# Optimization experiments

Measured on AMD Instinct MI355X. Metric: run time of the kernel, lower is better.

## Reference

```python
import jax, jax.numpy as jnp
import numpy as np

N_CB, VOCAB, CDIM = 8, 1024, 16
DECAY = 0.99
EPS = 1e-5


def setup_inputs() -> dict:
    key = jax.random.key(0)
    k1, k2, k3 = jax.random.split(key, 3)
    z = jax.random.normal(k1, (8, N_CB * CDIM, 32, 32), jnp.float32)
    codebooks = jax.random.normal(k2, (N_CB, VOCAB, CDIM), jnp.float32) * 0.02
    ema_count = jnp.zeros((N_CB, VOCAB), jnp.float32)
    ema_weight = jax.random.normal(k3, (N_CB, VOCAB, CDIM), jnp.float32) * 0.02
    return {"z": z, "codebooks": codebooks, "ema_count": ema_count, "ema_weight": ema_weight}


def reference(z, codebooks, ema_count, ema_weight):
    B, D, H, W = z.shape
    # (b d h w) -> (b h w, n_cb, cdim): matches rearrange + chunk(dim=-1)
    zp = z.transpose(0, 2, 3, 1).reshape(B * H * W, N_CB, CDIM)
    # squared distances (N, C, V): |z|^2 - 2 z.cb + |cb|^2
    d2 = (jnp.sum(zp * zp, axis=-1, keepdims=True)
          - 2.0 * jnp.einsum('ncd,cvd->ncv', zp, codebooks)
          + jnp.sum(codebooks * codebooks, axis=-1)[None, :, :])
    idx = jnp.argmin(d2, axis=-1)                      # (N, C) int
    zq = codebooks[jnp.arange(N_CB)[None, :], idx]     # (N, C, d) gather

    # --- EMA codebook update (training-mode math, no grad) ---
    idx_c = idx.T                                      # (C, N)
    zp_c = zp.transpose(1, 0, 2)                       # (C, N, d)
    counts = jax.vmap(lambda i: jnp.zeros((VOCAB,), jnp.float32).at[i].add(1.0))(idx_c)
    sums = jax.vmap(lambda i, x: jnp.zeros((VOCAB, CDIM), jnp.float32).at[i].add(x))(idx_c, zp_c)
    new_count = DECAY * ema_count + (1.0 - DECAY) * counts
    new_weight = DECAY * ema_weight + (1.0 - DECAY) * sums
    n = jnp.sum(new_count, axis=-1, keepdims=True)     # (C, 1)
    count = (new_count + EPS) / (n + VOCAB * EPS) * n  # Laplace-smoothed counts
    new_codebooks = new_weight / count[..., None]

    # commitment: mean over codebooks of per-part MSE == global MSE (equal part sizes)
    commitment = jnp.mean((zp - jax.lax.stop_gradient(zq)) ** 2)

    # straight-through estimator
    zq_st = zp + jax.lax.stop_gradient(zq - zp)        # (N, C, d)
    quantized = zq_st.reshape(B, H, W, D).transpose(0, 3, 1, 2)
    indices = idx.reshape(B, H, W, N_CB).transpose(0, 3, 1, 2)  # (B, C, H, W)
    return quantized, indices, commitment, new_codebooks, new_count, new_weight
```

## Files before the change

### kernel.cpp

```cpp
#include <hip/hip_runtime.h>


#define NCB   8
#define VOCAB 1024
#define CDIM  16
#define NPIX  8192
#define HW    1024

#define OFF_QUANT  0
#define OFF_IDX    1048576
#define OFF_COMMIT 1114112
#define OFF_NCB    1114113
#define OFF_NCNT   1245185
#define OFF_NWT    1253377

#define WS_COUNTS_OFF 0
#define WS_SUMS_OFF   (NCB * VOCAB)
#define WS_CARR_OFF   (NCB * VOCAB + NCB * VOCAB * CDIM)

__device__ __forceinline__ float npsum16(const float m[16]) {
#pragma clang fp contract(off)
  float r0 = m[0] + m[8];
  float r1 = m[1] + m[9];
  float r2 = m[2] + m[10];
  float r3 = m[3] + m[11];
  float r4 = m[4] + m[12];
  float r5 = m[5] + m[13];
  float r6 = m[6] + m[14];
  float r7 = m[7] + m[15];
  return ((r0 + r1) + (r2 + r3)) + ((r4 + r5) + (r6 + r7));
}

__device__ __forceinline__ float npsum16sq(const float a[16]) {
#pragma clang fp contract(off)
  float m[16];
#pragma unroll
  for (int d = 0; d < 16; ++d) m[d] = a[d] * a[d];
  return npsum16(m);
}

__device__ __forceinline__ void proc_entry(const float zv[16],
                                           const float e[16], float c2v,
                                           float z2, int idx, float& best,
                                           int& bi) {
#pragma clang fp contract(off)
  float m[16];
#pragma unroll
  for (int d = 0; d < 16; ++d) m[d] = zv[d] * e[d];
  float l0 = (m[0] + m[4]) + (m[8] + m[12]);
  float l1 = (m[1] + m[5]) + (m[9] + m[13]);
  float l2 = (m[2] + m[6]) + (m[10] + m[14]);
  float l3 = (m[3] + m[7]) + (m[11] + m[15]);
  const float dot = (l0 + l1) + (l2 + l3);
  const float d2 = (z2 - 2.0f * dot) + c2v;
  const bool lt = d2 < best;
  best = lt ? d2 : best;
  bi = lt ? idx : bi;
}

__global__ __launch_bounds__(512, 4) void k_assign(
    const float* __restrict__ z, const float* __restrict__ cb,
    float* __restrict__ out, float* __restrict__ ws_commit_arr) {
  __shared__ float s_c2[VOCAB];
  __shared__ float s_best[8 * 64];
  __shared__ int s_bi[8 * 64];

  const int c = blockIdx.x >> 7;
  const int pchunk = blockIdx.x & 127;
  const int t = threadIdx.x;
  const int pix = t & 63;
  const int w = t >> 6;
  const int wu = __builtin_amdgcn_readfirstlane(w);

  const float* cbc = cb + (size_t)c * VOCAB * CDIM;

  for (int v = t; v < VOCAB; v += 512) {
    float e[16];
#pragma unroll
    for (int d = 0; d < 16; ++d) e[d] = cbc[(size_t)v * CDIM + d];
    s_c2[v] = npsum16sq(e);
  }

  const int n = pchunk * 64 + pix;
  const int b = n >> 10;
  const int hw = n & 1023;

  const float* zbase = z + ((size_t)(b * 128 + c * 16)) * HW + hw;
  float zv[16];
#pragma unroll
  for (int d = 0; d < 16; ++d) zv[d] = zbase[(size_t)d * HW];

  const float z2 = npsum16sq(zv);

  __syncthreads();

  const int vbase = wu * 128;
  const float* ep = cbc + (size_t)vbase * CDIM;

  float best = INFINITY;
  int bi = 0;

#pragma unroll 2
  for (int k = 0; k < 128; k += 2) {
    float ea[16], eb[16];
#pragma unroll
    for (int d = 0; d < 16; ++d) ea[d] = ep[(size_t)k * CDIM + d];
#pragma unroll
    for (int d = 0; d < 16; ++d) eb[d] = ep[(size_t)(k + 1) * CDIM + d];
    const float cv0 = s_c2[vbase + k];
    const float cv1 = s_c2[vbase + k + 1];
    proc_entry(zv, ea, cv0, z2, vbase + k, best, bi);
    proc_entry(zv, eb, cv1, z2, vbase + k + 1, best, bi);
  }

  s_best[w * 64 + pix] = best;
  s_bi[w * 64 + pix] = bi;
  __syncthreads();

  if (t < 64) {
    best = s_best[t];
    bi = s_bi[t];
#pragma unroll
    for (int s = 1; s < 8; ++s) {
      const float ob = s_best[s * 64 + t];
      const int oi = s_bi[s * 64 + t];
      const bool take = (ob < best) || (ob == best && oi < bi);
      best = take ? ob : best;
      bi = take ? oi : bi;
    }

    const float* qe = cbc + (size_t)bi * CDIM;
    float comm = 0.f;
#pragma unroll
    for (int d = 0; d < 16; ++d) {
      float zq = qe[d];
      float diff, qst;
      {
#pragma clang fp contract(off)
        diff = zv[d] - zq;
        qst = zv[d] + (zq - zv[d]);
      }
      comm += diff * diff;
      out[OFF_QUANT + ((size_t)(b * 128 + c * 16 + d)) * HW + hw] = qst;
    }
    out[OFF_IDX + ((size_t)(b * NCB + c)) * HW + hw] = (float)bi;

#pragma unroll
    for (int off = 32; off; off >>= 1) comm += __shfl_down(comm, off);
    if (t == 0) ws_commit_arr[blockIdx.x] = comm;
  }
}

__global__ __launch_bounds__(1024) void k_stats(
    const float* __restrict__ z, const float* __restrict__ outbuf,
    float* __restrict__ ws_counts, float* __restrict__ ws_sums_t) {
  __shared__ float s_sum[VOCAB];
  __shared__ float s_cnt[VOCAB];
  const int c = blockIdx.x >> 4;
  const int d = blockIdx.x & 15;
  const int t = threadIdx.x;

  s_sum[t] = 0.f;
  if (d == 0) s_cnt[t] = 0.f;
  __syncthreads();

#pragma unroll
  for (int k = 0; k < 8; ++k) {
    const int bi = (int)outbuf[OFF_IDX + ((size_t)(k * NCB + c)) * HW + t];
    const float zval = z[((size_t)(k * 128 + c * 16 + d)) * HW + t];
    atomicAdd(&s_sum[bi], zval);
    if (d == 0) atomicAdd(&s_cnt[bi], 1.0f);
  }
  __syncthreads();

  ws_sums_t[((size_t)(c * CDIM + d)) * VOCAB + t] = s_sum[t];
  if (d == 0) ws_counts[c * VOCAB + t] = s_cnt[t];
}

__global__ __launch_bounds__(256) void k_update(
    const float* __restrict__ ema_count, const float* __restrict__ ema_weight,
    const float* __restrict__ ws_counts, const float* __restrict__ ws_sums_t,
    const float* __restrict__ ws_commit_arr, float* __restrict__ out) {
  const int c = blockIdx.x >> 3;
  const int part = blockIdx.x & 7;
  const int t = threadIdx.x;
  __shared__ float s_red[4];
  __shared__ float s_n;
  __shared__ double s_dred[4];

  float psum = 0.f;
#pragma unroll
  for (int k = 0; k < 4; ++k) {
    const int v = k * 256 + t;
    psum += 0.99f * ema_count[c * VOCAB + v] + 0.01f * ws_counts[c * VOCAB + v];
  }
#pragma unroll
  for (int off = 32; off; off >>= 1) psum += __shfl_down(psum, off);
  if ((t & 63) == 0) s_red[t >> 6] = psum;
  __syncthreads();
  if (t == 0) s_n = (s_red[0] + s_red[1]) + (s_red[2] + s_red[3]);
  __syncthreads();
  const float nsum = s_n;
  const float veps = 0.01024f;

  if (t < 128) {
    const int v = part * 128 + t;
    out[OFF_NCNT + c * VOCAB + v] =
        0.99f * ema_count[c * VOCAB + v] + 0.01f * ws_counts[c * VOCAB + v];
  }

#pragma unroll
  for (int k = 0; k < 8; ++k) {
    const int i = part * 2048 + k * 256 + t;
    const int v = i >> 4;
    const int d = i & 15;
    const float nc =
        0.99f * ema_count[c * VOCAB + v] + 0.01f * ws_counts[c * VOCAB + v];
    const float cnt = (nc + 1e-5f) / (nsum + veps) * nsum;
    const size_t gi = (size_t)c * VOCAB * CDIM + i;
    const float nw = 0.99f * ema_weight[gi] +
                     0.01f * ws_sums_t[((size_t)(c * CDIM + d)) * VOCAB + v];
    out[OFF_NWT + gi] = nw;
    out[OFF_NCB + gi] = nw / cnt;
  }

  if (blockIdx.x == 0) {
    double ps = 0.0;
#pragma unroll
    for (int k = 0; k < 4; ++k) ps += (double)ws_commit_arr[k * 256 + t];
#pragma unroll
    for (int off = 32; off; off >>= 1) ps += __shfl_down(ps, off);
    if ((t & 63) == 0) s_dred[t >> 6] = ps;
    __syncthreads();
    if (t == 0)
      out[OFF_COMMIT] =
          (float)(((s_dred[0] + s_dred[1]) + (s_dred[2] + s_dred[3])) /
                  1048576.0);
  }
}

extern "C" void kernel_launch(void* const* d_in, const int* in_sizes, int n_in,
                              void* d_out, int out_size, void* d_ws,
                              size_t ws_size, hipStream_t stream) {
  const float* z = (const float*)d_in[0];
  const float* codebooks = (const float*)d_in[1];
  const float* ema_count = (const float*)d_in[2];
  const float* ema_weight = (const float*)d_in[3];
  float* out = (float*)d_out;

  float* wsf = (float*)d_ws;
  float* ws_counts = wsf + WS_COUNTS_OFF;
  float* ws_sums_t = wsf + WS_SUMS_OFF;
  float* ws_commit_arr = wsf + WS_CARR_OFF;


  k_assign<<<dim3(1024), dim3(512), 0, stream>>>(z, codebooks, out,
                                                 ws_commit_arr);
  k_stats<<<dim3(128), dim3(1024), 0, stream>>>(z, out, ws_counts, ws_sums_t);
  k_update<<<dim3(64), dim3(256), 0, stream>>>(ema_count, ema_weight,
                                               ws_counts, ws_sums_t,
                                               ws_commit_arr, out);
}
```

Before: 143.8 us.

## Fuse histogram statistics and EMA update into one per-codebook kernel

Merges the stats and update kernels into a single kernel with one 1024-thread block per codebook. Each block builds counts and all 16 per-dimension sums in LDS, padded to a stride of 17 to reduce bank conflicts, then applies the EMA update directly from shared memory. This removes one kernel launch and the workspace round trip for counts and sums. In exchange, the work that used to be spread over 128 and 64 blocks now runs on only 8 blocks. Each block serially performs many LDS atomics and streams a large share of z, which could lengthen the tail.

Measured after the change: 300.1 us. 109% more time.

```diff
diff --git a/kernel.cpp b/kernel.cpp
--- a/kernel.cpp
+++ b/kernel.cpp
@@ -14,9 +14,7 @@
 #define OFF_NCNT   1245185
 #define OFF_NWT    1253377
 
-#define WS_COUNTS_OFF 0
-#define WS_SUMS_OFF   (NCB * VOCAB)
-#define WS_CARR_OFF   (NCB * VOCAB + NCB * VOCAB * CDIM)
+#define WS_CARR_OFF 0
 
 __device__ __forceinline__ float npsum16(const float m[16]) {
 #pragma clang fp contract(off)
@@ -151,91 +149,92 @@
   }
 }
 
-__global__ __launch_bounds__(1024) void k_stats(
+__global__ __launch_bounds__(1024) void k_statsupd(
     const float* __restrict__ z, const float* __restrict__ outbuf,
-    float* __restrict__ ws_counts, float* __restrict__ ws_sums_t) {
-  __shared__ float s_sum[VOCAB];
+    const float* __restrict__ ema_count, const float* __restrict__ ema_weight,
+    const float* __restrict__ ws_commit_arr, float* __restrict__ out) {
+  __shared__ float s_sum[VOCAB * 17];
   __shared__ float s_cnt[VOCAB];
-  const int c = blockIdx.x >> 4;
-  const int d = blockIdx.x & 15;
+  __shared__ float s_fred[16];
+  __shared__ float s_n;
+  __shared__ double s_dred[16];
+
+  const int c = blockIdx.x;
   const int t = threadIdx.x;
-
-  s_sum[t] = 0.f;
-  if (d == 0) s_cnt[t] = 0.f;
-  __syncthreads();
-
+  const int lane = t & 63;
+  const int wv = t >> 6;
+
+#pragma unroll
+  for (int j = 0; j < 17; ++j) s_sum[j * 1024 + t] = 0.f;
+  s_cnt[t] = 0.f;
+  __syncthreads();
+
+  int bidx[8];
+#pragma unroll
+  for (int k = 0; k < 8; ++k)
+    bidx[k] = (int)outbuf[OFF_IDX + ((size_t)(k * NCB + c)) * HW + t];
+
+  float zA[16], zB[16];
+#pragma unroll
+  for (int d = 0; d < 16; ++d) zA[d] = z[((size_t)(c * 16 + d)) * HW + t];
 #pragma unroll
   for (int k = 0; k < 8; ++k) {
-    const int bi = (int)outbuf[OFF_IDX + ((size_t)(k * NCB + c)) * HW + t];
-    const float zval = z[((size_t)(k * 128 + c * 16 + d)) * HW + t];
-    atomicAdd(&s_sum[bi], zval);
-    if (d == 0) atomicAdd(&s_cnt[bi], 1.0f);
-  }
-  __syncthreads();
-
-  ws_sums_t[((size_t)(c * CDIM + d)) * VOCAB + t] = s_sum[t];
-  if (d == 0) ws_counts[c * VOCAB + t] = s_cnt[t];
-}
-
-__global__ __launch_bounds__(256) void k_update(
-    const float* __restrict__ ema_count, const float* __restrict__ ema_weight,
-    const float* __restrict__ ws_counts, const float* __restrict__ ws_sums_t,
-    const float* __restrict__ ws_commit_arr, float* __restrict__ out) {
-  const int c = blockIdx.x >> 3;
-  const int part = blockIdx.x & 7;
-  const int t = threadIdx.x;
-  __shared__ float s_red[4];
-  __shared__ float s_n;
-  __shared__ double s_dred[4];
-
-  float psum = 0.f;
-#pragma unroll
-  for (int k = 0; k < 4; ++k) {
-    const int v = k * 256 + t;
-    psum += 0.99f * ema_count[c * VOCAB + v] + 0.01f * ws_counts[c * VOCAB + v];
-  }
+    if (k < 7) {
+#pragma unroll
+      for (int d = 0; d < 16; ++d)
+        zB[d] = z[((size_t)((k + 1) * 128 + c * 16 + d)) * HW + t];
+    }
+    const int bi = bidx[k];
+    atomicAdd(&s_cnt[bi], 1.0f);
+#pragma unroll
+    for (int d = 0; d < 16; ++d) atomicAdd(&s_sum[bi * 17 + d], zA[d]);
+#pragma unroll
+    for (int d = 0; d < 16; ++d) zA[d] = zB[d];
+  }
+  __syncthreads();
+
+  const float ncv = 0.99f * ema_count[c * VOCAB + t] + 0.01f * s_cnt[t];
+  out[OFF_NCNT + c * VOCAB + t] = ncv;
+  float psum = ncv;
 #pragma unroll
   for (int off = 32; off; off >>= 1) psum += __shfl_down(psum, off);
-  if ((t & 63) == 0) s_red[t >> 6] = psum;
-  __syncthreads();
-  if (t == 0) s_n = (s_red[0] + s_red[1]) + (s_red[2] + s_red[3]);
+  if (lane == 0) s_fred[wv] = psum;
+  __syncthreads();
+  if (t == 0) {
+    float s = 0.f;
+#pragma unroll
+    for (int i = 0; i < 16; ++i) s += s_fred[i];
+    s_n = s;
+  }
   __syncthreads();
   const float nsum = s_n;
   const float veps = 0.01024f;
 
-  if (t < 128) {
-    const int v = part * 128 + t;
-    out[OFF_NCNT + c * VOCAB + v] =
-        0.99f * ema_count[c * VOCAB + v] + 0.01f * ws_counts[c * VOCAB + v];
-  }
-
-#pragma unroll
-  for (int k = 0; k < 8; ++k) {
-    const int i = part * 2048 + k * 256 + t;
+#pragma unroll
+  for (int j = 0; j < 16; ++j) {
+    const int i = j * 1024 + t;
     const int v = i >> 4;
     const int d = i & 15;
-    const float nc =
-        0.99f * ema_count[c * VOCAB + v] + 0.01f * ws_counts[c * VOCAB + v];
+    const float nc = 0.99f * ema_count[c * VOCAB + v] + 0.01f * s_cnt[v];
     const float cnt = (nc + 1e-5f) / (nsum + veps) * nsum;
     const size_t gi = (size_t)c * VOCAB * CDIM + i;
-    const float nw = 0.99f * ema_weight[gi] +
-                     0.01f * ws_sums_t[((size_t)(c * CDIM + d)) * VOCAB + v];
+    const float nw = 0.99f * ema_weight[gi] + 0.01f * s_sum[v * 17 + d];
     out[OFF_NWT + gi] = nw;
     out[OFF_NCB + gi] = nw / cnt;
   }
 
-  if (blockIdx.x == 0) {
-    double ps = 0.0;
-#pragma unroll
-    for (int k = 0; k < 4; ++k) ps += (double)ws_commit_arr[k * 256 + t];
+  if (c == 0) {
+    double ps = (double)ws_commit_arr[t];
 #pragma unroll
     for (int off = 32; off; off >>= 1) ps += __shfl_down(ps, off);
-    if ((t & 63) == 0) s_dred[t >> 6] = ps;
+    if (lane == 0) s_dred[wv] = ps;
     __syncthreads();
-    if (t == 0)
-      out[OFF_COMMIT] =
-          (float)(((s_dred[0] + s_dred[1]) + (s_dred[2] + s_dred[3])) /
-                  1048576.0);
+    if (t == 0) {
+      double sd = 0.0;
+#pragma unroll
+      for (int i = 0; i < 16; ++i) sd += s_dred[i];
+      out[OFF_COMMIT] = (float)(sd / 1048576.0);
+    }
   }
 }
 
@@ -248,16 +247,12 @@
   const float* ema_weight = (const float*)d_in[3];
   float* out = (float*)d_out;
 
-  float* wsf = (float*)d_ws;
-  float* ws_counts = wsf + WS_COUNTS_OFF;
-  float* ws_sums_t = wsf + WS_SUMS_OFF;
-  float* ws_commit_arr = wsf + WS_CARR_OFF;
+  float* ws_commit_arr = (float*)d_ws + WS_CARR_OFF;
 
 
   k_assign<<<dim3(1024), dim3(512), 0, stream>>>(z, codebooks, out,
                                                  ws_commit_arr);
-  k_stats<<<dim3(128), dim3(1024), 0, stream>>>(z, out, ws_counts, ws_sums_t);
-  k_update<<<dim3(64), dim3(256), 0, stream>>>(ema_count, ema_weight,
-                                               ws_counts, ws_sums_t,
-                                               ws_commit_arr, out);
-}
+  k_statsupd<<<dim3(8), dim3(1024), 0, stream>>>(z, out, ema_count,
+                                                 ema_weight, ws_commit_arr,
+                                                 out);
+}
```
